# Kernel optimization log

Measured on AMD Instinct MI355X. Metric: run time of the kernel, lower is better.

Reference implementation:

```python
import jax, jax.numpy as jnp
import numpy as np

EPS = 1e-5  # torch nn.LayerNorm default


def _ln(x, g, b):
    m = jnp.mean(x, axis=-1, keepdims=True)
    v = jnp.mean(jnp.square(x - m), axis=-1, keepdims=True)
    return (x - m) * jax.lax.rsqrt(v + EPS) * g + b


def setup_inputs() -> dict:
    key = jax.random.key(0)
    ks = jax.random.split(key, 21)
    B, D, H, O = 32768, 512, 256, 128
    E, T, NS, NT, G = 10, 3, 4, 2, 64

    def rn(k, shape, s=0.02):
        return jax.random.normal(k, shape, jnp.float32) * s

    return dict(
        x=jax.random.normal(ks[0], (B, D), jnp.float32),
        ew1=rn(ks[1], (E, D, H)), eb1=rn(ks[2], (E, H)),
        eg1=1.0 + rn(ks[3], (E, H), 0.1), ebt1=rn(ks[4], (E, H), 0.1),
        ew2=rn(ks[5], (E, H, H)), eb2=rn(ks[6], (E, H)),
        eg2=1.0 + rn(ks[7], (E, H), 0.1), ebt2=rn(ks[8], (E, H), 0.1),
        ew3=rn(ks[9], (E, H, O)), eb3=rn(ks[10], (E, O)),
        eg3=1.0 + rn(ks[11], (E, O), 0.1), ebt3=rn(ks[12], (E, O), 0.1),
        tg_w1=rn(ks[13], (T, D, G)), tg_b1=rn(ks[14], (T, G)),
        tg_w2=rn(ks[15], (T, G, NS + NT)), tg_b2=rn(ks[16], (T, NS + NT)),
        sg_w1=rn(ks[17], (D, G)), sg_b1=rn(ks[18], (G,)),
        sg_w2=rn(ks[19], (G, E)), sg_b2=rn(ks[20], (E,)),
    )


def reference(x, ew1, eb1, eg1, ebt1, ew2, eb2, eg2, ebt2,
              ew3, eb3, eg3, ebt3, tg_w1, tg_b1, tg_w2, tg_b2,
              sg_w1, sg_b1, sg_w2, sg_b2):
    NS, NT, T = 4, 2, 3  # num_shared_experts, num_task_experts, num_tasks
    # Batched expert MLPs (eval mode: dropout is identity). eo: [E, B, O]
    h = jax.nn.relu(_ln(jnp.einsum('bd,edh->ebh', x, ew1) + eb1[:, None, :],
                        eg1[:, None, :], ebt1[:, None, :]))
    h = jax.nn.relu(_ln(jnp.einsum('ebh,ehk->ebk', h, ew2) + eb2[:, None, :],
                        eg2[:, None, :], ebt2[:, None, :]))
    eo = jax.nn.relu(_ln(jnp.einsum('ebh,eho->ebo', h, ew3) + eb3[:, None, :],
                         eg3[:, None, :], ebt3[:, None, :]))
    E, B, O = eo.shape
    shared = eo[:NS]                              # [NS, B, O]
    task_eo = eo[NS:].reshape(T, NT, B, O)        # [T, NT, B, O]

    # Per-task gates: softmax over NS+NT experts. gw: [T, B, NS+NT]
    gh = jax.nn.relu(jnp.einsum('bd,tdg->tbg', x, tg_w1) + tg_b1[:, None, :])
    gw = jax.nn.softmax(jnp.einsum('tbg,tge->tbe', gh, tg_w2) + tg_b2[:, None, :],
                        axis=-1)
    # combined: [T, NS+NT, B, O] (shared first, matching torch.cat order)
    combined = jnp.concatenate(
        [jnp.broadcast_to(shared[None], (T, NS, B, O)), task_eo], axis=1)
    task_out = jnp.einsum('tbe,tebo->tbo', gw, combined)  # [T, B, O]

    # Shared gate over all E experts (order: shared, task0, task1, task2)
    sgh = jax.nn.relu(x @ sg_w1 + sg_b1)
    sgw = jax.nn.softmax(sgh @ sg_w2 + sg_b2, axis=-1)    # [B, E]
    shared_out = jnp.einsum('be,ebo->bo', sgw, eo)        # [B, O]

    # Pack (task_final_outputs list, shared_output) as one [T+1, B, O] array
    return jnp.concatenate([task_out, shared_out[None]], axis=0)
```

## Files before the change

kernel.cpp:

```cpp
#include <hip/hip_runtime.h>
#include <math.h>

typedef __attribute__((ext_vector_type(8))) _Float16 half8;
typedef __attribute__((ext_vector_type(8))) short short8;
typedef __attribute__((ext_vector_type(4))) float float4v;

static __device__ __forceinline__ unsigned short f2h(float f) {
  union { _Float16 h; unsigned short u; } c;
  c.h = (_Float16)f;
  return c.u;
}
static __device__ __forceinline__ float h2f(unsigned short u) {
  union { unsigned short u; _Float16 h; } c;
  c.u = u;
  return (float)c.h;
}

static __device__ __forceinline__ void gload16(const unsigned short* g,
                                               unsigned short* l) {
  __builtin_amdgcn_global_load_lds(
      (const __attribute__((address_space(1))) unsigned int*)g,
      (__attribute__((address_space(3))) unsigned int*)l, 16, 0, 0);
}

__global__ __launch_bounds__(256)
void split_pack(const float* __restrict__ src, unsigned short* __restrict__ dh,
                unsigned short* __restrict__ dl, int K, int N) {
  __shared__ float t[32][33];
  src += (size_t)blockIdx.z * K * N;
  const size_t tsz = (size_t)N * 32;
  const size_t tb = ((size_t)blockIdx.z * (K >> 5) + blockIdx.x) * tsz;
  const int k0 = blockIdx.x * 32, n0 = blockIdx.y * 32;
  const int tid = threadIdx.x;
  const int r = tid >> 3, c4 = (tid & 7) * 4;

  const float4 v = *(const float4*)(src + (size_t)(k0 + r) * N + n0 + c4);
  t[r][c4 + 0] = v.x; t[r][c4 + 1] = v.y; t[r][c4 + 2] = v.z; t[r][c4 + 3] = v.w;
  __syncthreads();

  const int sel = tid >> 7;
  const int rl = (tid >> 2) & 31;
  const int qq = tid & 3;
  short8 vv;
  #pragma unroll
  for (int j = 0; j < 8; ++j) {
    const float f = t[qq * 8 + j][rl];
    const unsigned short hb = f2h(f);
    ((unsigned short*)&vv)[j] = sel ? f2h(f - h2f(hb)) : hb;
  }
  unsigned short* dst = (sel ? dl : dh) + tb +
      (size_t)(n0 + rl) * 32 + (qq ^ ((rl >> 1) & 3)) * 8;
  *(short8*)dst = vv;
}

template<int N, int NT>
// ... 20 lines not shown
        const float v = acc[s][t][r] + cb[t];
        s1 += v; s2 += v * v;
      }
      #pragma unroll
      for (int off = 1; off < 16; off <<= 1) {
        s1 += __shfl_xor(s1, off, 16);
        s2 += __shfl_xor(s2, off, 16);
      }
      if (m == 0) {
        sumP[s * 16 + q * 4 + r][w] = s1;
        sqP[s * 16 + q * 4 + r][w] = s2;
      }
    }
  __syncthreads();
  #pragma unroll
  for (int s = 0; s < 4; ++s)
    #pragma unroll
    for (int r = 0; r < 4; ++r) {
      const int row = s * 16 + q * 4 + r;
      const float S1 = sumP[row][0] + sumP[row][1] + sumP[row][2] + sumP[row][3];
      const float S2 = sqP[row][0] + sqP[row][1] + sqP[row][2] + sqP[row][3];
      const float mean = S1 * (1.f / N);
      const float var = S2 * (1.f / N) - mean * mean;
      const float inv = rsqrtf(var + 1e-5f);
      #pragma unroll
      for (int t = 0; t < NT; ++t) {
        const float o =
            fmaxf((acc[s][t][r] + cb[t] - mean) * inv * cg[t] + cbt[t], 0.f);
        dst[row * dstride + w * NW + t * 16 + m] = f2h(o);
      }
    }
  __syncthreads();
}

#define LAH 0
#define LAL 2048
#define LBH 4096
#define LBL 12288
#define HBUF 20480

__global__ __launch_bounds__(256, 2)
void expert_tower(const float* __restrict__ x,
                  const unsigned short* __restrict__ w1h,
                  const unsigned short* __restrict__ w1l,
                  const float* __restrict__ eb1, const float* __restrict__ eg1,
                  const float* __restrict__ ebt1,
                  const unsigned short* __restrict__ w2h,
                  const unsigned short* __restrict__ w2l,
                  const float* __restrict__ eb2, const float* __restrict__ eg2,
                  const float* __restrict__ ebt2,
                  const unsigned short* __restrict__ w3h,
                  const unsigned short* __restrict__ w3l,
                  const float* __restrict__ eb3, const float* __restrict__ eg3,
                  const float* __restrict__ ebt3,
                  unsigned short* __restrict__ eo, int B) {
  __shared__ __align__(16) unsigned short pool[37376];
  __shared__ float sumP[64][4];
  __shared__ float sqP[64][4];

  const int tid = threadIdx.x;
  const int w = tid >> 6, lane = tid & 63, m = lane & 15, q = lane >> 4;
  const int qs8 = (q ^ ((m >> 1) & 3)) * 8;
  const int wb = w * 512;
  const int m0 = blockIdx.x * 64;
  const int e = blockIdx.y;
  const int arow = tid >> 2, ap = tid & 3;
  const int aswz = arow * 32 + (ap ^ ((arow >> 1) & 3)) * 8;

  eb1 += (size_t)e * 256; eg1 += (size_t)e * 256; ebt1 += (size_t)e * 256;
  eb2 += (size_t)e * 256; eg2 += (size_t)e * 256; ebt2 += (size_t)e * 256;
  eb3 += (size_t)e * 128; eg3 += (size_t)e * 128; ebt3 += (size_t)e * 128;

  float4v acc[4][4];

  #pragma unroll
  for (int s = 0; s < 4; ++s)
    #pragma unroll
    for (int t = 0; t < 4; ++t) acc[s][t] = (float4v){0.f, 0.f, 0.f, 0.f};

  const float* xrow = x + (size_t)(m0 + arow) * 512 + ap * 8;
  float4 f0 = *(const float4*)xrow;
  float4 f1 = *(const float4*)(xrow + 4);

  for (int kt = 0; kt < 16; ++kt) {
    const float fv[8] = {f0.x, f0.y, f0.z, f0.w, f1.x, f1.y, f1.z, f1.w};
    half8 ra, rla;
    #pragma unroll
    for (int j = 0; j < 8; ++j) {
      const _Float16 hb = (_Float16)fv[j];
      ra[j] = hb;
      rla[j] = (_Float16)(fv[j] - (float)hb);
    }
    __syncthreads();
    const size_t tb = ((size_t)(e * 16 + kt)) * 8192 + tid * 8;
    #pragma unroll
    for (int i = 0; i < 4; ++i) {
      gload16(w1h + tb + i * 2048, pool + LBH + wb + i * 2048);
      gload16(w1l + tb + i * 2048, pool + LBL + wb + i * 2048);
    }
    *(half8*)(pool + LAH + aswz) = ra;
    *(half8*)(pool + LAL + aswz) = rla;
    const int ktn = (kt < 15) ? kt + 1 : 15;
    f0 = *(const float4*)(xrow + ktn * 32);
    f1 = *(const float4*)(xrow + ktn * 32 + 4);
    __syncthreads();

    half8 ah[4], al[4];
    #pragma unroll
    for (int s = 0; s < 4; ++s) {
      const int off = (s * 16 + m) * 32 + qs8;
      ah[s] = *(const half8*)(pool + LAH + off);
      al[s] = *(const half8*)(pool + LAL + off);
    }
    #pragma unroll
    for (int t = 0; t < 4; ++t) {
      const int boff = (w * 64 + t * 16 + m) * 32 + qs8;
      const half8 bh = *(const half8*)(pool + LBH + boff);
      const half8 bl = *(const half8*)(pool + LBL + boff);
      #pragma unroll
      for (int s = 0; s < 4; ++s) {
        acc[s][t] = __builtin_amdgcn_mfma_f32_16x16x32_f16(ah[s], bh, acc[s][t], 0, 0, 0);
        acc[s][t] = __builtin_amdgcn_mfma_f32_16x16x32_f16(al[s], bh, acc[s][t], 0, 0, 0);
        acc[s][t] = __builtin_amdgcn_mfma_f32_16x16x32_f16(ah[s], bl, acc[s][t], 0, 0, 0);
      }
    }
  }
  ln_store_f16<256, 4>(acc, w, m, q, eb1, eg1, ebt1, pool + HBUF, 264, sumP, sqP);

  #pragma unroll
  for (int s = 0; s < 4; ++s)
    #pragma unroll
    for (int t = 0; t < 4; ++t) acc[s][t] = (float4v){0.f, 0.f, 0.f, 0.f};

  for (int kt = 0; kt < 8; ++kt) {
    __syncthreads();
    const size_t tb = ((size_t)(e * 8 + kt)) * 8192 + tid * 8;
    #pragma unroll
    for (int i = 0; i < 4; ++i) {
      gload16(w2h + tb + i * 2048, pool + LBH + wb + i * 2048);
      gload16(w2l + tb + i * 2048, pool + LBL + wb + i * 2048);
    }
    __syncthreads();

    half8 ah[4];
    #pragma unroll
    for (int s = 0; s < 4; ++s)
      ah[s] = *(const half8*)(pool + HBUF + (s * 16 + m) * 264 + kt * 32 + q * 8);
    #pragma unroll
    for (int t = 0; t < 4; ++t) {
      const int boff = (w * 64 + t * 16 + m) * 32 + qs8;
      const half8 bh = *(const half8*)(pool + LBH + boff);
      const half8 bl = *(const half8*)(pool + LBL + boff);
      #pragma unroll
      for (int s = 0; s < 4; ++s) {
        acc[s][t] = __builtin_amdgcn_mfma_f32_16x16x32_f16(ah[s], bh, acc[s][t], 0, 0, 0);
        acc[s][t] = __builtin_amdgcn_mfma_f32_16x16x32_f16(ah[s], bl, acc[s][t], 0, 0, 0);
      }
    }
  }
  ln_store_f16<256, 4>(acc, w, m, q, eb2, eg2, ebt2, pool + HBUF, 264, sumP, sqP);

  #pragma unroll
  for (int s = 0; s < 4; ++s)
    #pragma unroll
    for (int t = 0; t < 2; ++t) acc[s][t] = (float4v){0.f, 0.f, 0.f, 0.f};

  for (int kt = 0; kt < 8; ++kt) {
    __syncthreads();
    const size_t tb = ((size_t)(e * 8 + kt)) * 4096 + tid * 8;
    #pragma unroll
    for (int i = 0; i < 2; ++i) {
      gload16(w3h + tb + i * 2048, pool + LBH + wb + i * 2048);
      gload16(w3l + tb + i * 2048, pool + LBL + wb + i * 2048);
    }
    __syncthreads();

    half8 ah[4];
    #pragma unroll
    for (int s = 0; s < 4; ++s)
      ah[s] = *(const half8*)(pool + HBUF + (s * 16 + m) * 264 + kt * 32 + q * 8);
    #pragma unroll
    for (int t = 0; t < 2; ++t) {
      const int boff = (w * 32 + t * 16 + m) * 32 + qs8;
      const half8 bh = *(const half8*)(pool + LBH + boff);
      const half8 bl = *(const half8*)(pool + LBL + boff);
      #pragma unroll
      for (int s = 0; s < 4; ++s) {
        acc[s][t] = __builtin_amdgcn_mfma_f32_16x16x32_f16(ah[s], bh, acc[s][t], 0, 0, 0);
        acc[s][t] = __builtin_amdgcn_mfma_f32_16x16x32_f16(ah[s], bl, acc[s][t], 0, 0, 0);
      }
    }
  }
  unsigned short* rp = pool;
  ln_store_f16<128, 2>(acc, w, m, q, eb3, eg3, ebt3, rp, 136, sumP, sqP);
  #pragma unroll
  for (int i = 0; i < 4; ++i) {
    const int c = tid + i * 256;
    const int rowc = c >> 4, c8 = c & 15;
    *(short8*)(eo + ((size_t)e * B + m0 + rowc) * 128 + c8 * 8) =
        *(const short8*)(rp + rowc * 136 + c8 * 8);
  }
}

__global__ __launch_bounds__(256, 2)
void gate_gemm(const float* __restrict__ x, const unsigned short* __restrict__ twh,
               const unsigned short* __restrict__ twl,
               const float* __restrict__ tg_b1, const float* __restrict__ sg_b1,
               float* __restrict__ gh, int B) {
  __shared__ __align__(16) unsigned short gp[8192];
  const int tid = threadIdx.x;
  const int w = tid >> 6, lane = tid & 63, m = lane & 15, q = lane >> 4;
  const int qs8 = (q ^ ((m >> 1) & 3)) * 8;
  const int wb = w * 512;
  const int m0 = blockIdx.x * 64;
  const int slice = blockIdx.y;
  const int arow = tid >> 2, ap = tid & 3;
  const int aswz = arow * 32 + (ap ^ ((arow >> 1) & 3)) * 8;
  const float* bias = (slice < 3) ? tg_b1 + (size_t)slice * 64 : sg_b1;

  float4v acc[4];
  #pragma unroll
  for (int s = 0; s < 4; ++s) acc[s] = (float4v){0.f, 0.f, 0.f, 0.f};

  const float* xrow = x + (size_t)(m0 + arow) * 512 + ap * 8;
  float4 f0 = *(const float4*)xrow;
  float4 f1 = *(const float4*)(xrow + 4);

  for (int kt = 0; kt < 16; ++kt) {
    const float fv[8] = {f0.x, f0.y, f0.z, f0.w, f1.x, f1.y, f1.z, f1.w};
    half8 ra, rla;
    #pragma unroll
    for (int j = 0; j < 8; ++j) {
      const _Float16 hb = (_Float16)fv[j];
      ra[j] = hb;
      rla[j] = (_Float16)(fv[j] - (float)hb);
    }
    __syncthreads();
    const size_t tb = ((size_t)(slice * 16 + kt)) * 2048 + tid * 8;
    gload16(twh + tb, gp + 4096 + wb);
    gload16(twl + tb, gp + 6144 + wb);
    *(half8*)(gp + aswz) = ra;
    *(half8*)(gp + 2048 + aswz) = rla;
    const int ktn = (kt < 15) ? kt + 1 : 15;
    f0 = *(const float4*)(xrow + ktn * 32);
    f1 = *(const float4*)(xrow + ktn * 32 + 4);
    __syncthreads();

    const int boff = (w * 16 + m) * 32 + qs8;
    const half8 bh = *(const half8*)(gp + 4096 + boff);
    const half8 bl = *(const half8*)(gp + 6144 + boff);
    #pragma unroll
    for (int s = 0; s < 4; ++s) {
      const int aoff = (s * 16 + m) * 32 + qs8;
      const half8 ah = *(const half8*)(gp + aoff);
      const half8 al = *(const half8*)(gp + 2048 + aoff);
      acc[s] = __builtin_amdgcn_mfma_f32_16x16x32_f16(ah, bh, acc[s], 0, 0, 0);
      acc[s] = __builtin_amdgcn_mfma_f32_16x16x32_f16(al, bh, acc[s], 0, 0, 0);
      acc[s] = __builtin_amdgcn_mfma_f32_16x16x32_f16(ah, bl, acc[s], 0, 0, 0);
    }
  }
  const float cb = bias[w * 16 + m];
  #pragma unroll
  for (int s = 0; s < 4; ++s)
    #pragma unroll
    for (int r = 0; r < 4; ++r) {
      const int row = m0 + s * 16 + q * 4 + r;
      gh[((size_t)slice * B + row) * 64 + w * 16 + m] =
          fmaxf(acc[s][r] + cb, 0.f);
    }
}

template<int NOUT>
__global__ __launch_bounds__(256)
void gate2(const float* __restrict__ gh, const float* __restrict__ w2,
           const float* __restrict__ b2, float* __restrict__ outw, int B) {
  const int b0 = blockIdx.x * 64;
  __shared__ float ghs[64][65];
  __shared__ float wls[64 * NOUT];
  __shared__ float bls[NOUT];
  const int tid = threadIdx.x;

  const float* src = gh + (size_t)b0 * 64;
  for (int f = tid; f < 64 * 16; f += 256) {
    const int r = f >> 4, c4 = f & 15;
    const float4 v = *(const float4*)(src + r * 64 + c4 * 4);
    ghs[r][c4 * 4 + 0] = v.x;
    ghs[r][c4 * 4 + 1] = v.y;
    ghs[r][c4 * 4 + 2] = v.z;
    ghs[r][c4 * 4 + 3] = v.w;
  }
  for (int f = tid; f < 64 * NOUT; f += 256) wls[f] = w2[f];
  if (tid < NOUT) bls[tid] = b2[tid];
  __syncthreads();

  if (tid < 64) {
    const int b = b0 + tid;
    float a[NOUT];
    #pragma unroll
    for (int n = 0; n < NOUT; ++n) a[n] = bls[n];
    for (int k = 0; k < 64; ++k) {
      const float g = ghs[tid][k];
      #pragma unroll
      for (int n = 0; n < NOUT; ++n) a[n] = fmaf(g, wls[k * NOUT + n], a[n]);
    }
    float mx = a[0];
    #pragma unroll
    for (int n = 1; n < NOUT; ++n) mx = fmaxf(mx, a[n]);
    float sum = 0.f;
    #pragma unroll
    for (int n = 0; n < NOUT; ++n) { a[n] = expf(a[n] - mx); sum += a[n]; }
    const float r = 1.f / sum;
    #pragma unroll
    for (int n = 0; n < NOUT; ++n) outw[(size_t)b * NOUT + n] = a[n] * r;
  }
}

__global__ __launch_bounds__(256)
void combine(const unsigned short* __restrict__ eo, const float* __restrict__ gw,
             const float* __restrict__ sgw, float* __restrict__ out, int B) {
  const int tid = threadIdx.x;
  const int gb = blockIdx.x * 16 + (tid >> 4);
  const int c0 = (tid & 15) * 8;

  float a[4][8];
  #pragma unroll
  for (int s = 0; s < 4; ++s)
    #pragma unroll
    for (int i = 0; i < 8; ++i) a[s][i] = 0.f;

  #pragma unroll
  for (int e = 0; e < 10; ++e) {
    const half8 vv = *(const half8*)(eo + ((size_t)e * B + gb) * 128 + c0);
    float f[8];
    #pragma unroll
    for (int i = 0; i < 8; ++i) f[i] = (float)vv[i];
    float c[4];
    c[3] = sgw[(size_t)gb * 10 + e];
    c[0] = c[1] = c[2] = 0.f;
    if (e < 4) {
      c[0] = gw[((size_t)0 * B + gb) * 6 + e];
      c[1] = gw[((size_t)1 * B + gb) * 6 + e];
      c[2] = gw[((size_t)2 * B + gb) * 6 + e];
    } else {
      const int tt = (e - 4) >> 1;
      c[tt] = gw[((size_t)tt * B + gb) * 6 + 4 + ((e - 4) & 1)];
    }
// ... 23 lines not shown
  const float* ebt1  = (const float*)d_in[4];
  const float* ew2   = (const float*)d_in[5];
  const float* eb2   = (const float*)d_in[6];
  const float* eg2   = (const float*)d_in[7];
  const float* ebt2  = (const float*)d_in[8];
  const float* ew3   = (const float*)d_in[9];
  const float* eb3   = (const float*)d_in[10];
  const float* eg3   = (const float*)d_in[11];
  const float* ebt3  = (const float*)d_in[12];
  const float* tg_w1 = (const float*)d_in[13];
  const float* tg_b1 = (const float*)d_in[14];
  const float* tg_w2 = (const float*)d_in[15];
  const float* tg_b2 = (const float*)d_in[16];
  const float* sg_w1 = (const float*)d_in[17];
  const float* sg_b1 = (const float*)d_in[18];
  const float* sg_w2 = (const float*)d_in[19];
  const float* sg_b2 = (const float*)d_in[20];
  float* out = (float*)d_out;

  const int B = 32768, D = 512, H = 256, O = 128, G = 64, E = 10;
  (void)D; (void)H; (void)O; (void)G;

  char* p = (char*)d_ws;
  unsigned short* w1h  = (unsigned short*)p; p += (size_t)E * 16 * 8192 * 2;
  unsigned short* w1l  = (unsigned short*)p; p += (size_t)E * 16 * 8192 * 2;
  unsigned short* w2h  = (unsigned short*)p; p += (size_t)E * 8 * 8192 * 2;
  unsigned short* w2l  = (unsigned short*)p; p += (size_t)E * 8 * 8192 * 2;
  unsigned short* w3h  = (unsigned short*)p; p += (size_t)E * 8 * 4096 * 2;
  unsigned short* w3l  = (unsigned short*)p; p += (size_t)E * 8 * 4096 * 2;
  unsigned short* twh  = (unsigned short*)p; p += (size_t)4 * 16 * 2048 * 2;
  unsigned short* twl  = (unsigned short*)p; p += (size_t)4 * 16 * 2048 * 2;
  float* gwb  = (float*)p; p += (size_t)3 * B * 6 * 4;
  float* sgwb = (float*)p; p += (size_t)B * 10 * 4;
  unsigned short* eo = (unsigned short*)p;
  float* gh = (float*)eo;

  split_pack<<<dim3(16, 8, E), 256, 0, stream>>>(ew1, w1h, w1l, 512, 256);
  split_pack<<<dim3(8, 8, E), 256, 0, stream>>>(ew2, w2h, w2l, 256, 256);
  split_pack<<<dim3(8, 4, E), 256, 0, stream>>>(ew3, w3h, w3l, 256, 128);
  split_pack<<<dim3(16, 2, 3), 256, 0, stream>>>(tg_w1, twh, twl, 512, 64);
  split_pack<<<dim3(16, 2, 1), 256, 0, stream>>>(
      sg_w1, twh + (size_t)3 * 16 * 2048, twl + (size_t)3 * 16 * 2048, 512, 64);

  gate_gemm<<<dim3(B / 64, 4), 256, 0, stream>>>(x, twh, twl, tg_b1, sg_b1,
                                                 gh, B);
  for (int t = 0; t < 3; ++t)
    gate2<6><<<B / 64, 256, 0, stream>>>(gh + (size_t)t * B * G,
                                         tg_w2 + (size_t)t * G * 6,
                                         tg_b2 + (size_t)t * 6,
                                         gwb + (size_t)t * B * 6, B);
  gate2<10><<<B / 64, 256, 0, stream>>>(gh + (size_t)3 * B * G, sg_w2, sg_b2,
                                        sgwb, B);

  expert_tower<<<dim3(B / 64, E), 256, 0, stream>>>(
      x, w1h, w1l, eb1, eg1, ebt1, w2h, w2l, eb2, eg2, ebt2,
      w3h, w3l, eb3, eg3, ebt3, eo, B);

  combine<<<B / 16, 256, 0, stream>>>(eo, gwb, sgwb, out, B);
}
```

Measured before the change: 763.7 us.

## Double-buffer LDS tiles and register-prefetch weights in expert and gate GEMMs

Layer-1 of expert_tower and gate_gemm now double-buffer both the split-fp16 x tile and the weight tiles in LDS. The next tile's async loads are issued before the current tile's MFMAs, and each iteration ends with one explicit wait plus barrier instead of two __syncthreads. Layers 2 and 3 prefetch the next weight tile into registers while computing the current one, replacing direct global-to-LDS loads. The intent is to hide global-load latency behind MFMA work. In exchange, LDS grows to 80 KB in expert_tower (which may limit it to fewer resident blocks per CU), register pressure rises, and gate_gemm's occupancy hint is raised to 4.

```diff
diff --git a/kernel.cpp b/kernel.cpp
--- a/kernel.cpp
+++ b/kernel.cpp
@@ -107,12 +107,6 @@
     }
   __syncthreads();
 }
-
-#define LAH 0
-#define LAL 2048
-#define LBH 4096
-#define LBL 12288
-#define HBUF 20480
 
 __global__ __launch_bounds__(256, 2)
 void expert_tower(const float* __restrict__ x,
@@ -129,9 +123,10 @@
                   const float* __restrict__ eb3, const float* __restrict__ eg3,
                   const float* __restrict__ ebt3,
                   unsigned short* __restrict__ eo, int B) {
-  __shared__ __align__(16) unsigned short pool[37376];
-  __shared__ float sumP[64][4];
-  __shared__ float sqP[64][4];
+  __shared__ __align__(16) unsigned short pool[40960];
+  float (*sumP)[4] = (float (*)[4])(pool + 16384);
+  float (*sqP)[4]  = (float (*)[4])(pool + 16896);
+  unsigned short* hbuf = pool + 24064;
 
   const int tid = threadIdx.x;
   const int w = tid >> 6, lane = tid & 63, m = lane & 15, q = lane >> 4;
@@ -157,7 +152,7 @@
   float4 f0 = *(const float4*)xrow;
   float4 f1 = *(const float4*)(xrow + 4);
 
-  for (int kt = 0; kt < 16; ++kt) {
+  {
     const float fv[8] = {f0.x, f0.y, f0.z, f0.w, f1.x, f1.y, f1.z, f1.w};
     half8 ra, rla;
     #pragma unroll
@@ -166,32 +161,62 @@
       ra[j] = hb;
       rla[j] = (_Float16)(fv[j] - (float)hb);
     }
-    __syncthreads();
-    const size_t tb = ((size_t)(e * 16 + kt)) * 8192 + tid * 8;
+    *(half8*)(pool + aswz) = ra;
+    *(half8*)(pool + 2048 + aswz) = rla;
+    const size_t tb = ((size_t)(e * 16)) * 8192 + tid * 8;
     #pragma unroll
     for (int i = 0; i < 4; ++i) {
-      gload16(w1h + tb + i * 2048, pool + LBH + wb + i * 2048);
-      gload16(w1l + tb + i * 2048, pool + LBL + wb + i * 2048);
-    }
-    *(half8*)(pool + LAH + aswz) = ra;
-    *(half8*)(pool + LAL + aswz) = rla;
-    const int ktn = (kt < 15) ? kt + 1 : 15;
-    f0 = *(const float4*)(xrow + ktn * 32);
-    f1 = *(const float4*)(xrow + ktn * 32 + 4);
-    __syncthreads();
-
+      gload16(w1h + tb + i * 2048, pool + 8192 + wb + i * 2048);
+      gload16(w1l + tb + i * 2048, pool + 8192 + 8192 + wb + i * 2048);
+    }
+    f0 = *(const float4*)(xrow + 32);
+    f1 = *(const float4*)(xrow + 36);
+    __builtin_amdgcn_sched_barrier(0);
+    asm volatile("s_waitcnt vmcnt(0) lgkmcnt(0)" ::: "memory");
+    __builtin_amdgcn_sched_barrier(0);
+    __builtin_amdgcn_s_barrier();
+  }
+
+  #pragma unroll 2
+  for (int kt = 0; kt < 16; ++kt) {
+    const int cur = kt & 1, nxt = cur ^ 1;
+    if (kt < 15) {
+      const float fv[8] = {f0.x, f0.y, f0.z, f0.w, f1.x, f1.y, f1.z, f1.w};
+      half8 ra, rla;
+      #pragma unroll
+      for (int j = 0; j < 8; ++j) {
+        const _Float16 hb = (_Float16)fv[j];
+        ra[j] = hb;
+        rla[j] = (_Float16)(fv[j] - (float)hb);
+      }
+      *(half8*)(pool + nxt * 4096 + aswz) = ra;
+      *(half8*)(pool + nxt * 4096 + 2048 + aswz) = rla;
+      const size_t tb = ((size_t)(e * 16 + kt + 1)) * 8192 + tid * 8;
+      #pragma unroll
+      for (int i = 0; i < 4; ++i) {
+        gload16(w1h + tb + i * 2048, pool + 8192 + nxt * 16384 + wb + i * 2048);
+        gload16(w1l + tb + i * 2048,
+                pool + 8192 + nxt * 16384 + 8192 + wb + i * 2048);
+      }
+      const int ktn = (kt < 14) ? kt + 2 : 15;
+      f0 = *(const float4*)(xrow + ktn * 32);
+      f1 = *(const float4*)(xrow + ktn * 32 + 4);
+      __builtin_amdgcn_sched_barrier(0);
+    }
     half8 ah[4], al[4];
+    const unsigned short* ab = pool + cur * 4096;
     #pragma unroll
     for (int s = 0; s < 4; ++s) {
       const int off = (s * 16 + m) * 32 + qs8;
-      ah[s] = *(const half8*)(pool + LAH + off);
-      al[s] = *(const half8*)(pool + LAL + off);
-    }
+      ah[s] = *(const half8*)(ab + off);
+      al[s] = *(const half8*)(ab + 2048 + off);
+    }
+    const unsigned short* bb = pool + 8192 + cur * 16384;
     #pragma unroll
     for (int t = 0; t < 4; ++t) {
       const int boff = (w * 64 + t * 16 + m) * 32 + qs8;
-      const half8 bh = *(const half8*)(pool + LBH + boff);
-      const half8 bl = *(const half8*)(pool + LBL + boff);
+      const half8 bh = *(const half8*)(bb + boff);
+      const half8 bl = *(const half8*)(bb + 8192 + boff);
       #pragma unroll
       for (int s = 0; s < 4; ++s) {
         acc[s][t] = __builtin_amdgcn_mfma_f32_16x16x32_f16(ah[s], bh, acc[s][t], 0, 0, 0);
@@ -199,33 +224,57 @@
         acc[s][t] = __builtin_amdgcn_mfma_f32_16x16x32_f16(ah[s], bl, acc[s][t], 0, 0, 0);
       }
     }
-  }
-  ln_store_f16<256, 4>(acc, w, m, q, eb1, eg1, ebt1, pool + HBUF, 264, sumP, sqP);
+    if (kt < 15) {
+      __builtin_amdgcn_sched_barrier(0);
+      asm volatile("s_waitcnt vmcnt(0)" ::: "memory");
+      __builtin_amdgcn_sched_barrier(0);
+      __builtin_amdgcn_s_barrier();
+    }
+  }
+  ln_store_f16<256, 4>(acc, w, m, q, eb1, eg1, ebt1, hbuf, 264, sumP, sqP);
 
   #pragma unroll
   for (int s = 0; s < 4; ++s)
     #pragma unroll
     for (int t = 0; t < 4; ++t) acc[s][t] = (float4v){0.f, 0.f, 0.f, 0.f};
 
+  short8 rh[4], rl[4];
+  {
+    const size_t tb = ((size_t)(e * 8)) * 8192 + tid * 8;
+    #pragma unroll
+    for (int i = 0; i < 4; ++i) {
+      rh[i] = *(const short8*)(w2h + tb + i * 2048);
+      rl[i] = *(const short8*)(w2l + tb + i * 2048);
+    }
+  }
   for (int kt = 0; kt < 8; ++kt) {
-    __syncthreads();
-    const size_t tb = ((size_t)(e * 8 + kt)) * 8192 + tid * 8;
+    if (kt) __builtin_amdgcn_s_barrier();
     #pragma unroll
     for (int i = 0; i < 4; ++i) {
-      gload16(w2h + tb + i * 2048, pool + LBH + wb + i * 2048);
-      gload16(w2l + tb + i * 2048, pool + LBL + wb + i * 2048);
-    }
-    __syncthreads();
-
+      *(short8*)(pool + i * 2048 + tid * 8) = rh[i];
+      *(short8*)(pool + 8192 + i * 2048 + tid * 8) = rl[i];
+    }
+    if (kt < 7) {
+      const size_t tb = ((size_t)(e * 8 + kt + 1)) * 8192 + tid * 8;
+      #pragma unroll
+      for (int i = 0; i < 4; ++i) {
+        rh[i] = *(const short8*)(w2h + tb + i * 2048);
+        rl[i] = *(const short8*)(w2l + tb + i * 2048);
+      }
+    }
+    __builtin_amdgcn_sched_barrier(0);
+    asm volatile("s_waitcnt lgkmcnt(0)" ::: "memory");
+    __builtin_amdgcn_sched_barrier(0);
+    __builtin_amdgcn_s_barrier();
     half8 ah[4];
     #pragma unroll
     for (int s = 0; s < 4; ++s)
-      ah[s] = *(const half8*)(pool + HBUF + (s * 16 + m) * 264 + kt * 32 + q * 8);
+      ah[s] = *(const half8*)(hbuf + (s * 16 + m) * 264 + kt * 32 + q * 8);
     #pragma unroll
     for (int t = 0; t < 4; ++t) {
       const int boff = (w * 64 + t * 16 + m) * 32 + qs8;
-      const half8 bh = *(const half8*)(pool + LBH + boff);
-      const half8 bl = *(const half8*)(pool + LBL + boff);
+      const half8 bh = *(const half8*)(pool + boff);
+      const half8 bl = *(const half8*)(pool + 8192 + boff);
       #pragma unroll
       for (int s = 0; s < 4; ++s) {
         acc[s][t] = __builtin_amdgcn_mfma_f32_16x16x32_f16(ah[s], bh, acc[s][t], 0, 0, 0);
@@ -233,32 +282,50 @@
       }
     }
   }
-  ln_store_f16<256, 4>(acc, w, m, q, eb2, eg2, ebt2, pool + HBUF, 264, sumP, sqP);
+  ln_store_f16<256, 4>(acc, w, m, q, eb2, eg2, ebt2, hbuf, 264, sumP, sqP);
 
   #pragma unroll
   for (int s = 0; s < 4; ++s)
     #pragma unroll
     for (int t = 0; t < 2; ++t) acc[s][t] = (float4v){0.f, 0.f, 0.f, 0.f};
 
+  short8 sh[2], sl[2];
+  {
+    const size_t tb = ((size_t)(e * 8)) * 4096 + tid * 8;
+    #pragma unroll
+    for (int i = 0; i < 2; ++i) {
+      sh[i] = *(const short8*)(w3h + tb + i * 2048);
+      sl[i] = *(const short8*)(w3l + tb + i * 2048);
+    }
+  }
   for (int kt = 0; kt < 8; ++kt) {
-    __syncthreads();
-    const size_t tb = ((size_t)(e * 8 + kt)) * 4096 + tid * 8;
+    if (kt) __builtin_amdgcn_s_barrier();
     #pragma unroll
     for (int i = 0; i < 2; ++i) {
-      gload16(w3h + tb + i * 2048, pool + LBH + wb + i * 2048);
-      gload16(w3l + tb + i * 2048, pool + LBL + wb + i * 2048);
-    }
-    __syncthreads();
-
+      *(short8*)(pool + i * 2048 + tid * 8) = sh[i];
+      *(short8*)(pool + 4096 + i * 2048 + tid * 8) = sl[i];
+    }
+    if (kt < 7) {
+      const size_t tb = ((size_t)(e * 8 + kt + 1)) * 4096 + tid * 8;
+      #pragma unroll
+      for (int i = 0; i < 2; ++i) {
+        sh[i] = *(const short8*)(w3h + tb + i * 2048);
+        sl[i] = *(const short8*)(w3l + tb + i * 2048);
+      }
+    }
+    __builtin_amdgcn_sched_barrier(0);
+    asm volatile("s_waitcnt lgkmcnt(0)" ::: "memory");
+    __builtin_amdgcn_sched_barrier(0);
+    __builtin_amdgcn_s_barrier();
     half8 ah[4];
     #pragma unroll
     for (int s = 0; s < 4; ++s)
-      ah[s] = *(const half8*)(pool + HBUF + (s * 16 + m) * 264 + kt * 32 + q * 8);
+      ah[s] = *(const half8*)(hbuf + (s * 16 + m) * 264 + kt * 32 + q * 8);
     #pragma unroll
     for (int t = 0; t < 2; ++t) {
       const int boff = (w * 32 + t * 16 + m) * 32 + qs8;
-      const half8 bh = *(const half8*)(pool + LBH + boff);
-      const half8 bl = *(const half8*)(pool + LBL + boff);
+      const half8 bh = *(const half8*)(pool + boff);
+      const half8 bl = *(const half8*)(pool + 4096 + boff);
       #pragma unroll
       for (int s = 0; s < 4; ++s) {
         acc[s][t] = __builtin_amdgcn_mfma_f32_16x16x32_f16(ah[s], bh, acc[s][t], 0, 0, 0);
@@ -277,12 +344,12 @@
   }
 }
 
-__global__ __launch_bounds__(256, 2)
+__global__ __launch_bounds__(256, 4)
 void gate_gemm(const float* __restrict__ x, const unsigned short* __restrict__ twh,
                const unsigned short* __restrict__ twl,
                const float* __restrict__ tg_b1, const float* __restrict__ sg_b1,
                float* __restrict__ gh, int B) {
-  __shared__ __align__(16) unsigned short gp[8192];
+  __shared__ __align__(16) unsigned short gp[16384];
   const int tid = threadIdx.x;
   const int w = tid >> 6, lane = tid & 63, m = lane & 15, q = lane >> 4;
   const int qs8 = (q ^ ((m >> 1) & 3)) * 8;
@@ -301,7 +368,7 @@
   float4 f0 = *(const float4*)xrow;
   float4 f1 = *(const float4*)(xrow + 4);
 
-  for (int kt = 0; kt < 16; ++kt) {
+  {
     const float fv[8] = {f0.x, f0.y, f0.z, f0.w, f1.x, f1.y, f1.z, f1.w};
     half8 ra, rla;
     #pragma unroll
@@ -310,28 +377,60 @@
       ra[j] = hb;
       rla[j] = (_Float16)(fv[j] - (float)hb);
     }
-    __syncthreads();
-    const size_t tb = ((size_t)(slice * 16 + kt)) * 2048 + tid * 8;
-    gload16(twh + tb, gp + 4096 + wb);
-    gload16(twl + tb, gp + 6144 + wb);
     *(half8*)(gp + aswz) = ra;
     *(half8*)(gp + 2048 + aswz) = rla;
-    const int ktn = (kt < 15) ? kt + 1 : 15;
-    f0 = *(const float4*)(xrow + ktn * 32);
-    f1 = *(const float4*)(xrow + ktn * 32 + 4);
-    __syncthreads();
-
+    const size_t tb = ((size_t)(slice * 16)) * 2048 + tid * 8;
+    gload16(twh + tb, gp + 8192 + wb);
+    gload16(twl + tb, gp + 8192 + 2048 + wb);
+    f0 = *(const float4*)(xrow + 32);
+    f1 = *(const float4*)(xrow + 36);
+    __builtin_amdgcn_sched_barrier(0);
+    asm volatile("s_waitcnt vmcnt(0) lgkmcnt(0)" ::: "memory");
+    __builtin_amdgcn_sched_barrier(0);
+    __builtin_amdgcn_s_barrier();
+  }
+
+  #pragma unroll 2
+  for (int kt = 0; kt < 16; ++kt) {
+    const int cur = kt & 1, nxt = cur ^ 1;
+    if (kt < 15) {
+      const float fv[8] = {f0.x, f0.y, f0.z, f0.w, f1.x, f1.y, f1.z, f1.w};
+      half8 ra, rla;
+      #pragma unroll
+      for (int j = 0; j < 8; ++j) {
+        const _Float16 hb = (_Float16)fv[j];
+        ra[j] = hb;
+        rla[j] = (_Float16)(fv[j] - (float)hb);
+      }
+      *(half8*)(gp + nxt * 4096 + aswz) = ra;
+      *(half8*)(gp + nxt * 4096 + 2048 + aswz) = rla;
+      const size_t tb = ((size_t)(slice * 16 + kt + 1)) * 2048 + tid * 8;
+      gload16(twh + tb, gp + 8192 + nxt * 4096 + wb);
+      gload16(twl + tb, gp + 8192 + nxt * 4096 + 2048 + wb);
+      const int ktn = (kt < 14) ? kt + 2 : 15;
+      f0 = *(const float4*)(xrow + ktn * 32);
+      f1 = *(const float4*)(xrow + ktn * 32 + 4);
+      __builtin_amdgcn_sched_barrier(0);
+    }
+    const unsigned short* ab = gp + cur * 4096;
+    const unsigned short* bb = gp + 8192 + cur * 4096;
     const int boff = (w * 16 + m) * 32 + qs8;
-    const half8 bh = *(const half8*)(gp + 4096 + boff);
-    const half8 bl = *(const half8*)(gp + 6144 + boff);
+    const half8 bh = *(const half8*)(bb + boff);
+    const half8 bl = *(const half8*)(bb + 2048 + boff);
     #pragma unroll
     for (int s = 0; s < 4; ++s) {
       const int aoff = (s * 16 + m) * 32 + qs8;
-      const half8 ah = *(const half8*)(gp + aoff);
-      const half8 al = *(const half8*)(gp + 2048 + aoff);
+      const half8 ah = *(const half8*)(ab + aoff);
+      const half8 al = *(const half8*)(ab + 2048 + aoff);
       acc[s] = __builtin_amdgcn_mfma_f32_16x16x32_f16(ah, bh, acc[s], 0, 0, 0);
       acc[s] = __builtin_amdgcn_mfma_f32_16x16x32_f16(al, bh, acc[s], 0, 0, 0);
       acc[s] = __builtin_amdgcn_mfma_f32_16x16x32_f16(ah, bl, acc[s], 0, 0, 0);
+    }
+    if (kt < 15) {
+      __builtin_amdgcn_sched_barrier(0);
+      asm volatile("s_waitcnt vmcnt(0)" ::: "memory");
+      __builtin_amdgcn_sched_barrier(0);
+      __builtin_amdgcn_s_barrier();
     }
   }
   const float cb = bias[w * 16 + m];
```

After: 768.5 us. No clear change (+0.6%).

## Pre-split x to fp16 pairs, load MFMA operands directly to registers with double buffering

Applied to the files above, without the earlier changes.

Adds a split_x kernel that converts x once into fp16 hi/lo arrays, so the expert and gate kernels no longer redo the conversion per expert. The expert tower and gate GEMMs drop their LDS staging and barriers for A and B tiles. They instead load operands straight from global into registers, prefetching the next k-step while the MFMAs run, and raise wave priority around the MFMA blocks. The gate first and second layers are fused into one kernel, removing the gh round trip and three launches. The cost is more register pressure, uncoalesced per-lane global loads that rely on cache, and extra workspace for xh/xl.

```diff
diff --git a/kernel.cpp b/kernel.cpp
--- a/kernel.cpp
+++ b/kernel.cpp
@@ -16,11 +16,22 @@
   return (float)c.h;
 }
 
-static __device__ __forceinline__ void gload16(const unsigned short* g,
-                                               unsigned short* l) {
-  __builtin_amdgcn_global_load_lds(
-      (const __attribute__((address_space(1))) unsigned int*)g,
-      (__attribute__((address_space(3))) unsigned int*)l, 16, 0, 0);
+__global__ __launch_bounds__(256)
+void split_x(const float* __restrict__ x, unsigned short* __restrict__ xh,
+             unsigned short* __restrict__ xl) {
+  const size_t i = ((size_t)blockIdx.x * 256 + threadIdx.x) * 8;
+  const float4 f0 = *(const float4*)(x + i);
+  const float4 f1 = *(const float4*)(x + i + 4);
+  const float fv[8] = {f0.x, f0.y, f0.z, f0.w, f1.x, f1.y, f1.z, f1.w};
+  half8 hh, ll;
+  #pragma unroll
+  for (int j = 0; j < 8; ++j) {
+    const _Float16 hb = (_Float16)fv[j];
+    hh[j] = hb;
+    ll[j] = (_Float16)(fv[j] - (float)hb);
+  }
+  *(half8*)(xh + i) = hh;
+  *(half8*)(xl + i) = ll;
 }
 
 __global__ __launch_bounds__(256)
@@ -108,14 +119,86 @@
   __syncthreads();
 }
 
-#define LAH 0
-#define LAL 2048
-#define LBH 4096
-#define LBL 12288
-#define HBUF 20480
+#define P1_STEP(KT, CAh, CAl, CBh, CBl, NAh, NAl, NBh, NBl)                    \
+  {                                                                            \
+    if ((KT) < 15) {                                                           \
+      const unsigned short* bp =                                               \
+          w1h + (size_t)(e * 16 + (KT) + 1) * 8192 + wB;                       \
+      const unsigned short* bq =                                               \
+          w1l + (size_t)(e * 16 + (KT) + 1) * 8192 + wB;                       \
+      _Pragma("unroll") for (int t = 0; t < 4; ++t) {                          \
+        NBh[t] = *(const half8*)(bp + t * 512);                                \
+        NBl[t] = *(const half8*)(bq + t * 512);                                \
+      }                                                                        \
+      _Pragma("unroll") for (int s = 0; s < 4; ++s) {                          \
+        NAh[s] = *(const half8*)(xph + s * 8192 + ((KT) + 1) * 32);            \
+        NAl[s] = *(const half8*)(xpl + s * 8192 + ((KT) + 1) * 32);            \
+      }                                                                        \
+    }                                                                          \
+    __builtin_amdgcn_s_setprio(1);                                             \
+    _Pragma("unroll") for (int t = 0; t < 4; ++t) {                            \
+      _Pragma("unroll") for (int s = 0; s < 4; ++s) {                          \
+        acc[s][t] = __builtin_amdgcn_mfma_f32_16x16x32_f16(CAh[s], CBh[t], acc[s][t], 0, 0, 0); \
+        acc[s][t] = __builtin_amdgcn_mfma_f32_16x16x32_f16(CAl[s], CBh[t], acc[s][t], 0, 0, 0); \
+        acc[s][t] = __builtin_amdgcn_mfma_f32_16x16x32_f16(CAh[s], CBl[t], acc[s][t], 0, 0, 0); \
+      }                                                                        \
+    }                                                                          \
+    __builtin_amdgcn_s_setprio(0);                                             \
+  }
+
+#define P2_STEP(KT, CBh, CBl, NBh, NBl)                                        \
+  {                                                                            \
+    if ((KT) < 7) {                                                            \
+      const unsigned short* bp =                                               \
+          w2h + (size_t)(e * 8 + (KT) + 1) * 8192 + wB;                        \
+      const unsigned short* bq =                                               \
+          w2l + (size_t)(e * 8 + (KT) + 1) * 8192 + wB;                        \
+      _Pragma("unroll") for (int t = 0; t < 4; ++t) {                          \
+        NBh[t] = *(const half8*)(bp + t * 512);                                \
+        NBl[t] = *(const half8*)(bq + t * 512);                                \
+      }                                                                        \
+    }                                                                          \
+    half8 ah[4];                                                               \
+    _Pragma("unroll") for (int s = 0; s < 4; ++s)                              \
+      ah[s] = *(const half8*)(hbuf + (s * 16 + m) * 264 + (KT) * 32 + q * 8);  \
+    __builtin_amdgcn_s_setprio(1);                                             \
+    _Pragma("unroll") for (int t = 0; t < 4; ++t) {                            \
+      _Pragma("unroll") for (int s = 0; s < 4; ++s) {                          \
+        acc[s][t] = __builtin_amdgcn_mfma_f32_16x16x32_f16(ah[s], CBh[t], acc[s][t], 0, 0, 0); \
+        acc[s][t] = __builtin_amdgcn_mfma_f32_16x16x32_f16(ah[s], CBl[t], acc[s][t], 0, 0, 0); \
+      }                                                                        \
+    }                                                                          \
+    __builtin_amdgcn_s_setprio(0);                                             \
+  }
+
+#define P3_STEP(KT, CBh, CBl, NBh, NBl)                                        \
+  {                                                                            \
+    if ((KT) < 7) {                                                            \
+      const unsigned short* bp =                                               \
+          w3h + (size_t)(e * 8 + (KT) + 1) * 4096 + wB3;                       \
+      const unsigned short* bq =                                               \
+          w3l + (size_t)(e * 8 + (KT) + 1) * 4096 + wB3;                       \
+      _Pragma("unroll") for (int t = 0; t < 2; ++t) {                          \
+        NBh[t] = *(const half8*)(bp + t * 512);                                \
+        NBl[t] = *(const half8*)(bq + t * 512);                                \
+      }                                                                        \
+    }                                                                          \
+    half8 ah[4];                                                               \
+    _Pragma("unroll") for (int s = 0; s < 4; ++s)                              \
+      ah[s] = *(const half8*)(hbuf + (s * 16 + m) * 264 + (KT) * 32 + q * 8);  \
+    __builtin_amdgcn_s_setprio(1);                                             \
+    _Pragma("unroll") for (int t = 0; t < 2; ++t) {                            \
+      _Pragma("unroll") for (int s = 0; s < 4; ++s) {                          \
+        acc[s][t] = __builtin_amdgcn_mfma_f32_16x16x32_f16(ah[s], CBh[t], acc[s][t], 0, 0, 0); \
+        acc[s][t] = __builtin_amdgcn_mfma_f32_16x16x32_f16(ah[s], CBl[t], acc[s][t], 0, 0, 0); \
+      }                                                                        \
+    }                                                                          \
+    __builtin_amdgcn_s_setprio(0);                                             \
+  }
 
 __global__ __launch_bounds__(256, 2)
-void expert_tower(const float* __restrict__ x,
+void expert_tower(const unsigned short* __restrict__ xh,
+                  const unsigned short* __restrict__ xl,
                   const unsigned short* __restrict__ w1h,
                   const unsigned short* __restrict__ w1l,
                   const float* __restrict__ eb1, const float* __restrict__ eg1,
@@ -129,18 +212,20 @@
                   const float* __restrict__ eb3, const float* __restrict__ eg3,
                   const float* __restrict__ ebt3,
                   unsigned short* __restrict__ eo, int B) {
-  __shared__ __align__(16) unsigned short pool[37376];
+  __shared__ __align__(16) unsigned short hbuf[16896];
   __shared__ float sumP[64][4];
   __shared__ float sqP[64][4];
 
   const int tid = threadIdx.x;
   const int w = tid >> 6, lane = tid & 63, m = lane & 15, q = lane >> 4;
   const int qs8 = (q ^ ((m >> 1) & 3)) * 8;
-  const int wb = w * 512;
   const int m0 = blockIdx.x * 64;
   const int e = blockIdx.y;
-  const int arow = tid >> 2, ap = tid & 3;
-  const int aswz = arow * 32 + (ap ^ ((arow >> 1) & 3)) * 8;
+
+  const unsigned short* xph = xh + (size_t)(m0 + m) * 512 + q * 8;
+  const unsigned short* xpl = xl + (size_t)(m0 + m) * 512 + q * 8;
+  const int wB = (w * 64 + m) * 32 + qs8;
+  const int wB3 = (w * 32 + m) * 32 + qs8;
 
   eb1 += (size_t)e * 256; eg1 += (size_t)e * 256; ebt1 += (size_t)e * 256;
   eb2 += (size_t)e * 256; eg2 += (size_t)e * 256; ebt2 += (size_t)e * 256;
@@ -153,120 +238,67 @@
     #pragma unroll
     for (int t = 0; t < 4; ++t) acc[s][t] = (float4v){0.f, 0.f, 0.f, 0.f};
 
-  const float* xrow = x + (size_t)(m0 + arow) * 512 + ap * 8;
-  float4 f0 = *(const float4*)xrow;
-  float4 f1 = *(const float4*)(xrow + 4);
-
-  for (int kt = 0; kt < 16; ++kt) {
-    const float fv[8] = {f0.x, f0.y, f0.z, f0.w, f1.x, f1.y, f1.z, f1.w};
-    half8 ra, rla;
-    #pragma unroll
-    for (int j = 0; j < 8; ++j) {
-      const _Float16 hb = (_Float16)fv[j];
-      ra[j] = hb;
-      rla[j] = (_Float16)(fv[j] - (float)hb);
-    }
-    __syncthreads();
-    const size_t tb = ((size_t)(e * 16 + kt)) * 8192 + tid * 8;
-    #pragma unroll
-    for (int i = 0; i < 4; ++i) {
-      gload16(w1h + tb + i * 2048, pool + LBH + wb + i * 2048);
-      gload16(w1l + tb + i * 2048, pool + LBL + wb + i * 2048);
-    }
-    *(half8*)(pool + LAH + aswz) = ra;
-    *(half8*)(pool + LAL + aswz) = rla;
-    const int ktn = (kt < 15) ? kt + 1 : 15;
-    f0 = *(const float4*)(xrow + ktn * 32);
-    f1 = *(const float4*)(xrow + ktn * 32 + 4);
-    __syncthreads();
-
-    half8 ah[4], al[4];
+  half8 A0h[4], A0l[4], B0h[4], B0l[4];
+  half8 A1h[4], A1l[4], B1h[4], B1l[4];
+  {
+    const unsigned short* bp = w1h + (size_t)(e * 16) * 8192 + wB;
+    const unsigned short* bq = w1l + (size_t)(e * 16) * 8192 + wB;
+    #pragma unroll
+    for (int t = 0; t < 4; ++t) {
+      B0h[t] = *(const half8*)(bp + t * 512);
+      B0l[t] = *(const half8*)(bq + t * 512);
+    }
     #pragma unroll
     for (int s = 0; s < 4; ++s) {
-      const int off = (s * 16 + m) * 32 + qs8;
-      ah[s] = *(const half8*)(pool + LAH + off);
-      al[s] = *(const half8*)(pool + LAL + off);
-    }
+      A0h[s] = *(const half8*)(xph + s * 8192);
+      A0l[s] = *(const half8*)(xpl + s * 8192);
+    }
+  }
+  for (int kt = 0; kt < 16; kt += 2) {
+    P1_STEP(kt,     A0h, A0l, B0h, B0l, A1h, A1l, B1h, B1l);
+    P1_STEP(kt + 1, A1h, A1l, B1h, B1l, A0h, A0l, B0h, B0l);
+  }
+  ln_store_f16<256, 4>(acc, w, m, q, eb1, eg1, ebt1, hbuf, 264, sumP, sqP);
+
+  #pragma unroll
+  for (int s = 0; s < 4; ++s)
+    #pragma unroll
+    for (int t = 0; t < 4; ++t) acc[s][t] = (float4v){0.f, 0.f, 0.f, 0.f};
+
+  {
+    const unsigned short* bp = w2h + (size_t)(e * 8) * 8192 + wB;
+    const unsigned short* bq = w2l + (size_t)(e * 8) * 8192 + wB;
     #pragma unroll
     for (int t = 0; t < 4; ++t) {
-      const int boff = (w * 64 + t * 16 + m) * 32 + qs8;
-      const half8 bh = *(const half8*)(pool + LBH + boff);
-      const half8 bl = *(const half8*)(pool + LBL + boff);
-      #pragma unroll
-      for (int s = 0; s < 4; ++s) {
-        acc[s][t] = __builtin_amdgcn_mfma_f32_16x16x32_f16(ah[s], bh, acc[s][t], 0, 0, 0);
-        acc[s][t] = __builtin_amdgcn_mfma_f32_16x16x32_f16(al[s], bh, acc[s][t], 0, 0, 0);
-        acc[s][t] = __builtin_amdgcn_mfma_f32_16x16x32_f16(ah[s], bl, acc[s][t], 0, 0, 0);
-      }
-    }
-  }
-  ln_store_f16<256, 4>(acc, w, m, q, eb1, eg1, ebt1, pool + HBUF, 264, sumP, sqP);
-
-  #pragma unroll
-  for (int s = 0; s < 4; ++s)
-    #pragma unroll
-    for (int t = 0; t < 4; ++t) acc[s][t] = (float4v){0.f, 0.f, 0.f, 0.f};
-
-  for (int kt = 0; kt < 8; ++kt) {
-    __syncthreads();
-    const size_t tb = ((size_t)(e * 8 + kt)) * 8192 + tid * 8;
-    #pragma unroll
-    for (int i = 0; i < 4; ++i) {
-      gload16(w2h + tb + i * 2048, pool + LBH + wb + i * 2048);
-      gload16(w2l + tb + i * 2048, pool + LBL + wb + i * 2048);
-    }
-    __syncthreads();
-
-    half8 ah[4];
-    #pragma unroll
-    for (int s = 0; s < 4; ++s)
-      ah[s] = *(const half8*)(pool + HBUF + (s * 16 + m) * 264 + kt * 32 + q * 8);
-    #pragma unroll
-    for (int t = 0; t < 4; ++t) {
-      const int boff = (w * 64 + t * 16 + m) * 32 + qs8;
-      const half8 bh = *(const half8*)(pool + LBH + boff);
-      const half8 bl = *(const half8*)(pool + LBL + boff);
-      #pragma unroll
-      for (int s = 0; s < 4; ++s) {
-        acc[s][t] = __builtin_amdgcn_mfma_f32_16x16x32_f16(ah[s], bh, acc[s][t], 0, 0, 0);
-        acc[s][t] = __builtin_amdgcn_mfma_f32_16x16x32_f16(ah[s], bl, acc[s][t], 0, 0, 0);
-      }
-    }
-  }
-  ln_store_f16<256, 4>(acc, w, m, q, eb2, eg2, ebt2, pool + HBUF, 264, sumP, sqP);
+      B0h[t] = *(const half8*)(bp + t * 512);
+      B0l[t] = *(const half8*)(bq + t * 512);
+    }
+  }
+  for (int kt = 0; kt < 8; kt += 2) {
+    P2_STEP(kt,     B0h, B0l, B1h, B1l);
+    P2_STEP(kt + 1, B1h, B1l, B0h, B0l);
+  }
+  ln_store_f16<256, 4>(acc, w, m, q, eb2, eg2, ebt2, hbuf, 264, sumP, sqP);
 
   #pragma unroll
   for (int s = 0; s < 4; ++s)
     #pragma unroll
     for (int t = 0; t < 2; ++t) acc[s][t] = (float4v){0.f, 0.f, 0.f, 0.f};
 
-  for (int kt = 0; kt < 8; ++kt) {
-    __syncthreads();
-    const size_t tb = ((size_t)(e * 8 + kt)) * 4096 + tid * 8;
-    #pragma unroll
-    for (int i = 0; i < 2; ++i) {
-      gload16(w3h + tb + i * 2048, pool + LBH + wb + i * 2048);
-      gload16(w3l + tb + i * 2048, pool + LBL + wb + i * 2048);
-    }
-    __syncthreads();
-
-    half8 ah[4];
-    #pragma unroll
-    for (int s = 0; s < 4; ++s)
-      ah[s] = *(const half8*)(pool + HBUF + (s * 16 + m) * 264 + kt * 32 + q * 8);
+  {
+    const unsigned short* bp = w3h + (size_t)(e * 8) * 4096 + wB3;
+    const unsigned short* bq = w3l + (size_t)(e * 8) * 4096 + wB3;
     #pragma unroll
     for (int t = 0; t < 2; ++t) {
-      const int boff = (w * 32 + t * 16 + m) * 32 + qs8;
-      const half8 bh = *(const half8*)(pool + LBH + boff);
-      const half8 bl = *(const half8*)(pool + LBL + boff);
-      #pragma unroll
-      for (int s = 0; s < 4; ++s) {
-        acc[s][t] = __builtin_amdgcn_mfma_f32_16x16x32_f16(ah[s], bh, acc[s][t], 0, 0, 0);
-        acc[s][t] = __builtin_amdgcn_mfma_f32_16x16x32_f16(ah[s], bl, acc[s][t], 0, 0, 0);
-      }
-    }
-  }
-  unsigned short* rp = pool;
+      B0h[t] = *(const half8*)(bp + t * 512);
+      B0l[t] = *(const half8*)(bq + t * 512);
+    }
+  }
+  for (int kt = 0; kt < 8; kt += 2) {
+    P3_STEP(kt,     B0h, B0l, B1h, B1l);
+    P3_STEP(kt + 1, B1h, B1l, B0h, B0l);
+  }
+  unsigned short* rp = hbuf;
   ln_store_f16<128, 2>(acc, w, m, q, eb3, eg3, ebt3, rp, 136, sumP, sqP);
   #pragma unroll
   for (int i = 0; i < 4; ++i) {
@@ -277,99 +309,84 @@
   }
 }
 
-__global__ __launch_bounds__(256, 2)
-void gate_gemm(const float* __restrict__ x, const unsigned short* __restrict__ twh,
+#define G_STEP(KT, CAh, CAl, CBh, CBl, NAh, NAl, NBh, NBl)                     \
+  {                                                                            \
+    if ((KT) < 15) {                                                           \
+      const size_t tb = (size_t)(slice * 16 + (KT) + 1) * 2048 + wB;           \
+      NBh = *(const half8*)(twh + tb);                                         \
+      NBl = *(const half8*)(twl + tb);                                         \
+      _Pragma("unroll") for (int s = 0; s < 4; ++s) {                          \
+        NAh[s] = *(const half8*)(xph + s * 8192 + ((KT) + 1) * 32);            \
+        NAl[s] = *(const half8*)(xpl + s * 8192 + ((KT) + 1) * 32);            \
+      }                                                                        \
+    }                                                                          \
+    __builtin_amdgcn_s_setprio(1);                                             \
+    _Pragma("unroll") for (int s = 0; s < 4; ++s) {                            \
+      acc[s] = __builtin_amdgcn_mfma_f32_16x16x32_f16(CAh[s], CBh, acc[s], 0, 0, 0); \
+      acc[s] = __builtin_amdgcn_mfma_f32_16x16x32_f16(CAl[s], CBh, acc[s], 0, 0, 0); \
+      acc[s] = __builtin_amdgcn_mfma_f32_16x16x32_f16(CAh[s], CBl, acc[s], 0, 0, 0); \
+    }                                                                          \
+    __builtin_amdgcn_s_setprio(0);                                             \
+  }
+
+template<int NOUT>
+__global__ __launch_bounds__(256, 4)
+void gate_gemm(const unsigned short* __restrict__ xh,
+               const unsigned short* __restrict__ xl,
+               const unsigned short* __restrict__ twh,
                const unsigned short* __restrict__ twl,
-               const float* __restrict__ tg_b1, const float* __restrict__ sg_b1,
-               float* __restrict__ gh, int B) {
-  __shared__ __align__(16) unsigned short gp[8192];
+               const float* __restrict__ b1, const float* __restrict__ w2,
+               const float* __restrict__ b2, float* __restrict__ outw,
+               int slice_base, int B) {
+  __shared__ float ghs[64][65];
+  __shared__ float wls[64 * NOUT];
+  __shared__ float bls[NOUT];
+
   const int tid = threadIdx.x;
   const int w = tid >> 6, lane = tid & 63, m = lane & 15, q = lane >> 4;
   const int qs8 = (q ^ ((m >> 1) & 3)) * 8;
-  const int wb = w * 512;
   const int m0 = blockIdx.x * 64;
-  const int slice = blockIdx.y;
-  const int arow = tid >> 2, ap = tid & 3;
-  const int aswz = arow * 32 + (ap ^ ((arow >> 1) & 3)) * 8;
-  const float* bias = (slice < 3) ? tg_b1 + (size_t)slice * 64 : sg_b1;
+  const int slice = slice_base + blockIdx.y;
+  const unsigned short* xph = xh + (size_t)(m0 + m) * 512 + q * 8;
+  const unsigned short* xpl = xl + (size_t)(m0 + m) * 512 + q * 8;
+  const int wB = (w * 16 + m) * 32 + qs8;
+  const float* bias = b1 + (size_t)blockIdx.y * 64;
+  const float* w2p = w2 + (size_t)blockIdx.y * 64 * NOUT;
+  const float* b2p = b2 + (size_t)blockIdx.y * NOUT;
+  float* outp = outw + (size_t)blockIdx.y * B * NOUT;
 
   float4v acc[4];
   #pragma unroll
   for (int s = 0; s < 4; ++s) acc[s] = (float4v){0.f, 0.f, 0.f, 0.f};
 
-  const float* xrow = x + (size_t)(m0 + arow) * 512 + ap * 8;
-  float4 f0 = *(const float4*)xrow;
-  float4 f1 = *(const float4*)(xrow + 4);
-
-  for (int kt = 0; kt < 16; ++kt) {
-    const float fv[8] = {f0.x, f0.y, f0.z, f0.w, f1.x, f1.y, f1.z, f1.w};
-    half8 ra, rla;
-    #pragma unroll
-    for (int j = 0; j < 8; ++j) {
-      const _Float16 hb = (_Float16)fv[j];
-      ra[j] = hb;
-      rla[j] = (_Float16)(fv[j] - (float)hb);
-    }
-    __syncthreads();
-    const size_t tb = ((size_t)(slice * 16 + kt)) * 2048 + tid * 8;
-    gload16(twh + tb, gp + 4096 + wb);
-    gload16(twl + tb, gp + 6144 + wb);
-    *(half8*)(gp + aswz) = ra;
-    *(half8*)(gp + 2048 + aswz) = rla;
-    const int ktn = (kt < 15) ? kt + 1 : 15;
-    f0 = *(const float4*)(xrow + ktn * 32);
-    f1 = *(const float4*)(xrow + ktn * 32 + 4);
-    __syncthreads();
-
-    const int boff = (w * 16 + m) * 32 + qs8;
-    const half8 bh = *(const half8*)(gp + 4096 + boff);
-    const half8 bl = *(const half8*)(gp + 6144 + boff);
+  half8 A0h[4], A0l[4], A1h[4], A1l[4];
+  half8 B0h, B0l, B1h, B1l;
+  {
+    const size_t tb = (size_t)(slice * 16) * 2048 + wB;
+    B0h = *(const half8*)(twh + tb);
+    B0l = *(const half8*)(twl + tb);
     #pragma unroll
     for (int s = 0; s < 4; ++s) {
-      const int aoff = (s * 16 + m) * 32 + qs8;
-      const half8 ah = *(const half8*)(gp + aoff);
-      const half8 al = *(const half8*)(gp + 2048 + aoff);
-      acc[s] = __builtin_amdgcn_mfma_f32_16x16x32_f16(ah, bh, acc[s], 0, 0, 0);
-      acc[s] = __builtin_amdgcn_mfma_f32_16x16x32_f16(al, bh, acc[s], 0, 0, 0);
-      acc[s] = __builtin_amdgcn_mfma_f32_16x16x32_f16(ah, bl, acc[s], 0, 0, 0);
-    }
-  }
+      A0h[s] = *(const half8*)(xph + s * 8192);
+      A0l[s] = *(const half8*)(xpl + s * 8192);
+    }
+  }
+  for (int kt = 0; kt < 16; kt += 2) {
+    G_STEP(kt,     A0h, A0l, B0h, B0l, A1h, A1l, B1h, B1l);
+    G_STEP(kt + 1, A1h, A1l, B1h, B1l, A0h, A0l, B0h, B0l);
+  }
+
   const float cb = bias[w * 16 + m];
   #pragma unroll
   for (int s = 0; s < 4; ++s)
     #pragma unroll
-    for (int r = 0; r < 4; ++r) {
-      const int row = m0 + s * 16 + q * 4 + r;
-      gh[((size_t)slice * B + row) * 64 + w * 16 + m] =
-          fmaxf(acc[s][r] + cb, 0.f);
-    }
-}
-
-template<int NOUT>
-__global__ __launch_bounds__(256)
-void gate2(const float* __restrict__ gh, const float* __restrict__ w2,
-           const float* __restrict__ b2, float* __restrict__ outw, int B) {
-  const int b0 = blockIdx.x * 64;
-  __shared__ float ghs[64][65];
-  __shared__ float wls[64 * NOUT];
-  __shared__ float bls[NOUT];
-  const int tid = threadIdx.x;
-
-  const float* src = gh + (size_t)b0 * 64;
-  for (int f = tid; f < 64 * 16; f += 256) {
-    const int r = f >> 4, c4 = f & 15;
-    const float4 v = *(const float4*)(src + r * 64 + c4 * 4);
-    ghs[r][c4 * 4 + 0] = v.x;
-    ghs[r][c4 * 4 + 1] = v.y;
-    ghs[r][c4 * 4 + 2] = v.z;
-    ghs[r][c4 * 4 + 3] = v.w;
-  }
-  for (int f = tid; f < 64 * NOUT; f += 256) wls[f] = w2[f];
-  if (tid < NOUT) bls[tid] = b2[tid];
+    for (int r = 0; r < 4; ++r)
+      ghs[s * 16 + q * 4 + r][w * 16 + m] = fmaxf(acc[s][r] + cb, 0.f);
+  for (int f = tid; f < 64 * NOUT; f += 256) wls[f] = w2p[f];
+  if (tid < NOUT) bls[tid] = b2p[tid];
   __syncthreads();
 
   if (tid < 64) {
-    const int b = b0 + tid;
     float a[NOUT];
     #pragma unroll
     for (int n = 0; n < NOUT; ++n) a[n] = bls[n];
@@ -386,7 +403,8 @@
     for (int n = 0; n < NOUT; ++n) { a[n] = expf(a[n] - mx); sum += a[n]; }
     const float r = 1.f / sum;
     #pragma unroll
-    for (int n = 0; n < NOUT; ++n) outw[(size_t)b * NOUT + n] = a[n] * r;
+    for (int n = 0; n < NOUT; ++n)
+      outp[(size_t)(m0 + tid) * NOUT + n] = a[n] * r;
   }
 }
 
@@ -476,9 +494,11 @@
   unsigned short* twl  = (unsigned short*)p; p += (size_t)4 * 16 * 2048 * 2;
   float* gwb  = (float*)p; p += (size_t)3 * B * 6 * 4;
   float* sgwb = (float*)p; p += (size_t)B * 10 * 4;
-  unsigned short* eo = (unsigned short*)p;
-  float* gh = (float*)eo;
-
+  unsigned short* eo = (unsigned short*)p; p += (size_t)E * B * 128 * 2;
+  unsigned short* xh = (unsigned short*)p; p += (size_t)B * 512 * 2;
+  unsigned short* xl = (unsigned short*)p;
+
+  split_x<<<B * 512 / (256 * 8), 256, 0, stream>>>(x, xh, xl);
   split_pack<<<dim3(16, 8, E), 256, 0, stream>>>(ew1, w1h, w1l, 512, 256);
   split_pack<<<dim3(8, 8, E), 256, 0, stream>>>(ew2, w2h, w2l, 256, 256);
   split_pack<<<dim3(8, 4, E), 256, 0, stream>>>(ew3, w3h, w3l, 256, 128);
@@ -486,18 +506,13 @@
   split_pack<<<dim3(16, 2, 1), 256, 0, stream>>>(
       sg_w1, twh + (size_t)3 * 16 * 2048, twl + (size_t)3 * 16 * 2048, 512, 64);
 
-  gate_gemm<<<dim3(B / 64, 4), 256, 0, stream>>>(x, twh, twl, tg_b1, sg_b1,
-                                                 gh, B);
-  for (int t = 0; t < 3; ++t)
-    gate2<6><<<B / 64, 256, 0, stream>>>(gh + (size_t)t * B * G,
-                                         tg_w2 + (size_t)t * G * 6,
-                                         tg_b2 + (size_t)t * 6,
-                                         gwb + (size_t)t * B * 6, B);
-  gate2<10><<<B / 64, 256, 0, stream>>>(gh + (size_t)3 * B * G, sg_w2, sg_b2,
-                                        sgwb, B);
+  gate_gemm<6><<<dim3(B / 64, 3), 256, 0, stream>>>(
+      xh, xl, twh, twl, tg_b1, tg_w2, tg_b2, gwb, 0, B);
+  gate_gemm<10><<<dim3(B / 64, 1), 256, 0, stream>>>(
+      xh, xl, twh, twl, sg_b1, sg_w2, sg_b2, sgwb, 3, B);
 
   expert_tower<<<dim3(B / 64, E), 256, 0, stream>>>(
-      x, w1h, w1l, eb1, eg1, ebt1, w2h, w2l, eb2, eg2, ebt2,
+      xh, xl, w1h, w1l, eb1, eg1, ebt1, w2h, w2l, eb2, eg2, ebt2,
       w3h, w3l, eb3, eg3, ebt3, eo, B);
 
   combine<<<B / 16, 256, 0, stream>>>(eo, gwb, sgwb, out, B);
```

New measurement: 825.5 us. 8.1% more time.
